# Kernel tuning notes

Hardware: AMD Instinct MI355X
Metric: run time of the kernel (lower is better)

The kernel has to match this reference:

```python
import jax, jax.numpy as jnp
import numpy as np

MAX_SPIKE_TIME = 100.0
TH = 1.0
BIT = 8
K = 3
PAD = 1
OUT_CH = 64


def _unfold3x3(x):
    # torch F.unfold(kernel=3, padding=1, stride=1): output (B, C*9, H*W),
    # feature order channel-major then (kh, kw).
    B, C, H, W = x.shape
    xp = jnp.pad(x, ((0, 0), (0, 0), (PAD, PAD), (PAD, PAD)))
    cols = [xp[:, :, i:i + H, j:j + W] for i in range(K) for j in range(K)]
    p = jnp.stack(cols, axis=2)            # (B, C, 9, H, W)
    return p.reshape(B, C * K * K, H * W)  # (B, C*9, L)


def _weight_quantization(w):
    # tanh -> scale by global abs-max (no grad through alpha) -> round with STE
    w = jnp.tanh(w)
    alpha = jax.lax.stop_gradient(jnp.max(jnp.abs(w)))
    qmax = float(2 ** (BIT - 1) - 1)
    w = jnp.clip(w / alpha, -1.0, 1.0) * qmax
    w_hat = jax.lax.stop_gradient(jnp.round(w) - w) + w
    return w_hat * alpha / qmax


def _t_linear_c(patches, weight):
    # patches: (B, L, F_in); weight: (F_out, F_in)
    sorted_inp = jnp.sort(patches, axis=-1)      # (B, L, F_in)
    indic = jnp.argsort(patches, axis=-1)        # (B, L, F_in)
    wT = weight.T                                # (F_in, F_out)
    w_sorted = wT[indic]                         # (B, L, F_in, F_out)
    wq = _weight_quantization(w_sorted)
    si = sorted_inp[..., None]                   # (B, L, F_in, 1)
    weight_input_mul = si * wq
    weight_sum = jnp.cumsum(wq, axis=-2)
    input_weight_sum = jnp.cumsum(weight_input_mul, axis=-2)
    out_all = input_weight_sum / jnp.clip(weight_sum - TH, 1e-10, 1e10)
    out_spike = jnp.where(weight_sum < TH, MAX_SPIKE_TIME, out_all)
    out_spike = jnp.where(out_spike < si, MAX_SPIKE_TIME, out_spike)
    # causality check against the NEXT sorted input time (1.0 for the last slot)
    next_in = jnp.concatenate([si[..., 1:, :], jnp.ones_like(si[..., :1, :])], axis=-2)
    out_spike = jnp.where(out_spike > next_in, MAX_SPIKE_TIME, out_spike)
    return jnp.min(out_spike, axis=-2)           # (B, L, F_out)


def setup_inputs() -> dict:
    key = jax.random.key(0)
    k1, k2 = jax.random.split(key)
    inp = jax.random.uniform(k1, (4, 16, 32, 32), dtype=jnp.float32)
    in_features = K * K * 16
    weight = jax.random.uniform(k2, (OUT_CH, in_features), dtype=jnp.float32) * (10.0 / in_features)
    return {"inp": inp, "weight": weight}


def reference(inp, weight):
    B, C, H, W = inp.shape
    patches = _unfold3x3(inp).transpose(0, 2, 1)          # (B, L, F_in)
    patches = jnp.where(patches < 0.1, MAX_SPIKE_TIME, patches)
    out = _t_linear_c(patches, weight)                    # (B, L, F_out)
    out = out.transpose(0, 2, 1).reshape(B, OUT_CH, H, W)  # stride=1, pad=1 -> same HW
    return out
```

## Files before the change

### kernel.cpp

```cpp
#include <hip/hip_runtime.h>
#include <math.h>

constexpr int F_IN   = 144;
constexpr int F_OUT  = 64;
constexpr int H_IMG  = 32;
constexpr int W_IMG  = 32;
constexpr int NPIX   = 4 * H_IMG * W_IMG;
constexpr int PPB    = 8;
constexpr int NTHR   = PPB * 64;
#define MAX_SPIKE 100.0f

__global__ __launch_bounds__(256) void quant_fused_kernel(
    const float* __restrict__ w,
    float* __restrict__ wqT)
{
#pragma clang fp contract(off)
    __shared__ float wred[4];
    const int tid = threadIdx.x;

    float m = 0.f;
    {
        const float4* w4 = (const float4*)w;
        for (int i = tid; i < (F_OUT * F_IN) / 4; i += 256) {
            const float4 v = w4[i];
            m = fmaxf(m, fmaxf(fmaxf(fabsf(v.x), fabsf(v.y)),
                               fmaxf(fabsf(v.z), fabsf(v.w))));
        }
    }
    for (int s = 32; s > 0; s >>= 1)
        m = fmaxf(m, __shfl_xor(m, s, 64));
    if ((tid & 63) == 0) wred[tid >> 6] = m;
    __syncthreads();
    const float mw = fmaxf(fmaxf(wred[0], wred[1]), fmaxf(wred[2], wred[3]));
    const float alpha = tanhf(mw);

    const int i = blockIdx.x * 256 + tid;
    const int o = i / F_IN;
    const int f = i - o * F_IN;
    const float t = tanhf(w[i]);
    float x = t / alpha;
    x = fminf(fmaxf(x, -1.f), 1.f) * 127.f;
    const float r = rintf(x);
    wqT[f * F_OUT + o] = r * alpha / 127.f;
}

__global__ __launch_bounds__(NTHR, 4) void spike_conv_kernel(
    const float* __restrict__ inp,
    const float* __restrict__ wq,
    float* __restrict__ out)
{
#pragma clang fp contract(off)
    __shared__ __align__(16) float wql[F_IN * F_OUT];
    __shared__ __align__(16) unsigned long long kr[PPB][F_IN];
    __shared__ float sv[PPB][F_IN + 1];

    const int tid  = threadIdx.x;
    const int lane = tid & 63;
    const int wv_i = tid >> 6;
    const int p    = blockIdx.x * PPB + wv_i;
    const int b    = p >> 10;
    const int l    = p & 1023;
    const int h    = l >> 5;
    const int w    = l & 31;

    for (int c = wv_i; c < 36; c += PPB) {
        const float* g = wq + c * 256 + lane * 4;
        __builtin_amdgcn_global_load_lds(
            (const __attribute__((address_space(1))) void*)g,
            (__attribute__((address_space(3))) void*)&wql[c * 256],
            16, 0, 0);
    }

    float v0f, v1f, v2f;
    unsigned long long key0, key1, key2;
    {
        int idx[3] = { lane, lane + 64, lane + 128 };
        float vals[3];
        for (int m = 0; m < 3; ++m) {
            const int i = idx[m];
            float v = MAX_SPIKE;
            if (i < F_IN) {
                const int c  = i / 9;
                const int r  = i - c * 9;
                const int kh = r / 3;
                const int kw = r - kh * 3;
                const int hh = h + kh - 1;
                const int ww = w + kw - 1;
                float x = 0.f;
                if (hh >= 0 && hh < H_IMG && ww >= 0 && ww < W_IMG)
                    x = inp[((b * 16 + c) * H_IMG + hh) * W_IMG + ww];
                v = (x < 0.1f) ? MAX_SPIKE : x;
                kr[wv_i][i] = ((unsigned long long)__float_as_uint(v) << 8)
                              | (unsigned)i;
            }
            vals[m] = v;
        }
        v0f = vals[0]; v1f = vals[1]; v2f = vals[2];
        key0 = ((unsigned long long)__float_as_uint(v0f) << 8) | (unsigned)idx[0];
        key1 = ((unsigned long long)__float_as_uint(v1f) << 8) | (unsigned)idx[1];
        key2 = ((unsigned long long)__float_as_uint(v2f) << 8) | (unsigned)idx[2];
        if (lane == 0) sv[wv_i][F_IN] = 1.0f;
    }

    int r0 = 0, r1 = 0, r2 = 0;
    {
        const ulonglong2* ks2 = (const ulonglong2*)&kr[wv_i][0];
#pragma unroll 4
        for (int j = 0; j < F_IN / 2; ++j) {
            const ulonglong2 kk = ks2[j];
            r0 += (kk.x < key0) + (kk.y < key0);
            r1 += (kk.x < key1) + (kk.y < key1);
            r2 += (kk.x < key2) + (kk.y < key2);
        }
    }

    {
        unsigned* krlo = (unsigned*)&kr[wv_i][0];
        sv[wv_i][r0] = v0f;  krlo[2 * r0] = (unsigned)lane << 6;
        sv[wv_i][r1] = v1f;  krlo[2 * r1] = (unsigned)(lane + 64) << 6;
        if (lane < F_IN - 128) {
            sv[wv_i][r2] = v2f;  krlo[2 * r2] = (unsigned)(lane + 128) << 6;
        }
    }

    {
        unsigned* krhi = (unsigned*)&kr[wv_i][0];
        for (int k = lane; k < F_IN; k += 64)
            krhi[2 * k + 1] = __float_as_uint(sv[wv_i][k + 1]);
    }

    __syncthreads();

    float s   = sv[wv_i][0];
    float ws  = 0.f;
    float iws = 0.f;
    float mn  = MAX_SPIKE;
    bool  done = false;
    const ulonglong2* rec2 = (const ulonglong2*)&kr[wv_i][0];
    for (int k0 = 0; k0 < F_IN; k0 += 8) {
        if (s >= MAX_SPIKE) break;
        const ulonglong2 ra = rec2[(k0 >> 1) + 0];
        const ulonglong2 rb = rec2[(k0 >> 1) + 1];
        const ulonglong2 rc = rec2[(k0 >> 1) + 2];
        const ulonglong2 rd = rec2[(k0 >> 1) + 3];
        const unsigned long long r8[8] = { ra.x, ra.y, rb.x, rb.y,
                                           rc.x, rc.y, rd.x, rd.y };
        float su[8], nx[8], wsu[8], iwsu[8];
#pragma unroll
        for (int u = 0; u < 8; ++u) {
            su[u] = s;
            nx[u] = __uint_as_float((unsigned)(r8[u] >> 32));
            const float wvv = wql[(unsigned)r8[u] + lane];
            ws += wvv;
            const float prod = su[u] * wvv;
            iws += prod;
            wsu[u]  = ws;
            iwsu[u] = iws;
            s = nx[u];
        }
        if (!__all(wsu[7] < 1.0f)) {
#pragma unroll
            for (int u = 0; u < 8; ++u) {
                const float d = fmaxf(wsu[u] - 1.0f, 1e-10f);
                const float q = iwsu[u] / d;
                const bool valid = (wsu[u] >= 1.0f) & (q >= su[u]) & (q <= nx[u]);
                if (valid & !done) { mn = q; done = true; }
            }
            if (__all(done)) break;
        }
    }
    out[(b * F_OUT + lane) * 1024 + l] = mn;
}

extern "C" void kernel_launch(void* const* d_in, const int* in_sizes, int n_in,
                              void* d_out, int out_size, void* d_ws, size_t ws_size,
                              hipStream_t stream) {
    const float* inp = (const float*)d_in[0];
    const float* w   = (const float*)d_in[1];
    float* out = (float*)d_out;
    float* wqT = (float*)d_ws;

    quant_fused_kernel<<<36, 256, 0, stream>>>(w, wqT);
    spike_conv_kernel<<<NPIX / PPB, NTHR, 0, stream>>>(inp, wqT, out);
}
```

Measured before the change: 80.06 us.

## Fuse weight quantization into spike conv kernel, recomputing per block

Removes the separate quantization kernel launch and its workspace round trip. Each block now loads the raw weights into registers (18 per thread), reduces the global abs-max across its waves, applies tanh, quantizes, and writes the transposed result into shared memory. This saves one launch and the dependency between kernels, but every one of the 512 blocks redoes the full weight tanh and quantization work and an extra block-wide reduction.

```diff
diff --git a/kernel.cpp b/kernel.cpp
--- a/kernel.cpp
+++ b/kernel.cpp
@@ -8,51 +8,19 @@
 constexpr int NPIX   = 4 * H_IMG * W_IMG;
 constexpr int PPB    = 8;
 constexpr int NTHR   = PPB * 64;
+constexpr int WPT    = F_IN / PPB;
 #define MAX_SPIKE 100.0f
 
-__global__ __launch_bounds__(256) void quant_fused_kernel(
+__global__ __launch_bounds__(NTHR, 4) void spike_conv_fused(
+    const float* __restrict__ inp,
     const float* __restrict__ w,
-    float* __restrict__ wqT)
-{
-#pragma clang fp contract(off)
-    __shared__ float wred[4];
-    const int tid = threadIdx.x;
-
-    float m = 0.f;
-    {
-        const float4* w4 = (const float4*)w;
-        for (int i = tid; i < (F_OUT * F_IN) / 4; i += 256) {
-            const float4 v = w4[i];
-            m = fmaxf(m, fmaxf(fmaxf(fabsf(v.x), fabsf(v.y)),
-                               fmaxf(fabsf(v.z), fabsf(v.w))));
-        }
-    }
-    for (int s = 32; s > 0; s >>= 1)
-        m = fmaxf(m, __shfl_xor(m, s, 64));
-    if ((tid & 63) == 0) wred[tid >> 6] = m;
-    __syncthreads();
-    const float mw = fmaxf(fmaxf(wred[0], wred[1]), fmaxf(wred[2], wred[3]));
-    const float alpha = tanhf(mw);
-
-    const int i = blockIdx.x * 256 + tid;
-    const int o = i / F_IN;
-    const int f = i - o * F_IN;
-    const float t = tanhf(w[i]);
-    float x = t / alpha;
-    x = fminf(fmaxf(x, -1.f), 1.f) * 127.f;
-    const float r = rintf(x);
-    wqT[f * F_OUT + o] = r * alpha / 127.f;
-}
-
-__global__ __launch_bounds__(NTHR, 4) void spike_conv_kernel(
-    const float* __restrict__ inp,
-    const float* __restrict__ wq,
     float* __restrict__ out)
 {
 #pragma clang fp contract(off)
     __shared__ __align__(16) float wql[F_IN * F_OUT];
     __shared__ __align__(16) unsigned long long kr[PPB][F_IN];
     __shared__ float sv[PPB][F_IN + 1];
+    __shared__ float wred[PPB];
 
     const int tid  = threadIdx.x;
     const int lane = tid & 63;
@@ -61,14 +29,18 @@
     const int b    = p >> 10;
     const int l    = p & 1023;
     const int h    = l >> 5;
-    const int w    = l & 31;
+    const int wcol = l & 31;
 
-    for (int c = wv_i; c < 36; c += PPB) {
-        const float* g = wq + c * 256 + lane * 4;
-        __builtin_amdgcn_global_load_lds(
-            (const __attribute__((address_space(1))) void*)g,
-            (__attribute__((address_space(3))) void*)&wql[c * 256],
-            16, 0, 0);
+    const int fbase = wv_i * WPT;
+    float wreg[WPT];
+    {
+        const float2* g2 = (const float2*)(w + lane * F_IN + fbase);
+#pragma unroll
+        for (int k2 = 0; k2 < WPT / 2; ++k2) {
+            const float2 v = g2[k2];
+            wreg[2 * k2]     = v.x;
+            wreg[2 * k2 + 1] = v.y;
+        }
     }
 
     float v0f, v1f, v2f;
@@ -76,8 +48,8 @@
     {
         int idx[3] = { lane, lane + 64, lane + 128 };
         float vals[3];
-        for (int m = 0; m < 3; ++m) {
-            const int i = idx[m];
+        for (int m2 = 0; m2 < 3; ++m2) {
+            const int i = idx[m2];
             float v = MAX_SPIKE;
             if (i < F_IN) {
                 const int c  = i / 9;
@@ -85,7 +57,7 @@
                 const int kh = r / 3;
                 const int kw = r - kh * 3;
                 const int hh = h + kh - 1;
-                const int ww = w + kw - 1;
+                const int ww = wcol + kw - 1;
                 float x = 0.f;
                 if (hh >= 0 && hh < H_IMG && ww >= 0 && ww < W_IMG)
                     x = inp[((b * 16 + c) * H_IMG + hh) * W_IMG + ww];
@@ -93,7 +65,7 @@
                 kr[wv_i][i] = ((unsigned long long)__float_as_uint(v) << 8)
                               | (unsigned)i;
             }
-            vals[m] = v;
+            vals[m2] = v;
         }
         v0f = vals[0]; v1f = vals[1]; v2f = vals[2];
         key0 = ((unsigned long long)__float_as_uint(v0f) << 8) | (unsigned)idx[0];
@@ -129,6 +101,26 @@
             krhi[2 * k + 1] = __float_as_uint(sv[wv_i][k + 1]);
     }
 
+    float m = 0.f;
+#pragma unroll
+    for (int k = 0; k < WPT; ++k) m = fmaxf(m, fabsf(wreg[k]));
+    for (int s = 32; s > 0; s >>= 1)
+        m = fmaxf(m, __shfl_xor(m, s, 64));
+    if (lane == 0) wred[wv_i] = m;
+    __syncthreads();
+    float mw = wred[0];
+#pragma unroll
+    for (int q = 1; q < PPB; ++q) mw = fmaxf(mw, wred[q]);
+    const float alpha = tanhf(mw);
+
+#pragma unroll
+    for (int k = 0; k < WPT; ++k) {
+        const float t = tanhf(wreg[k]);
+        float x = t / alpha;
+        x = fminf(fmaxf(x, -1.f), 1.f) * 127.f;
+        const float r = rintf(x);
+        wql[(fbase + k) * F_OUT + lane] = r * alpha / 127.f;
+    }
     __syncthreads();
 
     float s   = sv[wv_i][0];
@@ -178,8 +170,7 @@
     const float* inp = (const float*)d_in[0];
     const float* w   = (const float*)d_in[1];
     float* out = (float*)d_out;
-    float* wqT = (float*)d_ws;
+    (void)d_ws; (void)ws_size;
 
-    quant_fused_kernel<<<36, 256, 0, stream>>>(w, wqT);
-    spike_conv_kernel<<<NPIX / PPB, NTHR, 0, stream>>>(inp, wqT, out);
+    spike_conv_fused<<<NPIX / PPB, NTHR, 0, stream>>>(inp, w, out);
 }
```

Result: no change. 81.64 us (+2.0%).

## Read quantized weights from global/L1 instead of staging them in LDS

Applied to the files above, without the earlier changes.

The scan kernel no longer copies the 36 KB quantized weight matrix into shared memory per block. Weight lookups now read global memory directly, relying on L1/L2 caching of the small table. This removes the block-wide barrier and shrinks LDS use, so more blocks can stay resident. Pixels per block drop from 8 to 4 and the rank-counting loop is unrolled by hand. The cost is that the data-dependent gathers now have global-memory latency instead of LDS latency.

```diff
diff --git a/kernel.cpp b/kernel.cpp
--- a/kernel.cpp
+++ b/kernel.cpp
@@ -6,11 +6,11 @@
 constexpr int H_IMG  = 32;
 constexpr int W_IMG  = 32;
 constexpr int NPIX   = 4 * H_IMG * W_IMG;
-constexpr int PPB    = 8;
+constexpr int PPB    = 4;
 constexpr int NTHR   = PPB * 64;
 #define MAX_SPIKE 100.0f
 
-__global__ __launch_bounds__(256) void quant_fused_kernel(
+__global__ __launch_bounds__(256) void quant_kernel(
     const float* __restrict__ w,
     float* __restrict__ wqT)
 {
@@ -44,13 +44,12 @@
     wqT[f * F_OUT + o] = r * alpha / 127.f;
 }
 
-__global__ __launch_bounds__(NTHR, 4) void spike_conv_kernel(
+__global__ __launch_bounds__(NTHR, 4) void spike_scan_kernel(
     const float* __restrict__ inp,
     const float* __restrict__ wq,
     float* __restrict__ out)
 {
 #pragma clang fp contract(off)
-    __shared__ __align__(16) float wql[F_IN * F_OUT];
     __shared__ __align__(16) unsigned long long kr[PPB][F_IN];
     __shared__ float sv[PPB][F_IN + 1];
 
@@ -61,23 +60,15 @@
     const int b    = p >> 10;
     const int l    = p & 1023;
     const int h    = l >> 5;
-    const int w    = l & 31;
-
-    for (int c = wv_i; c < 36; c += PPB) {
-        const float* g = wq + c * 256 + lane * 4;
-        __builtin_amdgcn_global_load_lds(
-            (const __attribute__((address_space(1))) void*)g,
-            (__attribute__((address_space(3))) void*)&wql[c * 256],
-            16, 0, 0);
-    }
+    const int wcol = l & 31;
 
     float v0f, v1f, v2f;
     unsigned long long key0, key1, key2;
     {
         int idx[3] = { lane, lane + 64, lane + 128 };
         float vals[3];
-        for (int m = 0; m < 3; ++m) {
-            const int i = idx[m];
+        for (int m2 = 0; m2 < 3; ++m2) {
+            const int i = idx[m2];
             float v = MAX_SPIKE;
             if (i < F_IN) {
                 const int c  = i / 9;
@@ -85,7 +76,7 @@
                 const int kh = r / 3;
                 const int kw = r - kh * 3;
                 const int hh = h + kh - 1;
-                const int ww = w + kw - 1;
+                const int ww = wcol + kw - 1;
                 float x = 0.f;
                 if (hh >= 0 && hh < H_IMG && ww >= 0 && ww < W_IMG)
                     x = inp[((b * 16 + c) * H_IMG + hh) * W_IMG + ww];
@@ -93,7 +84,7 @@
                 kr[wv_i][i] = ((unsigned long long)__float_as_uint(v) << 8)
                               | (unsigned)i;
             }
-            vals[m] = v;
+            vals[m2] = v;
         }
         v0f = vals[0]; v1f = vals[1]; v2f = vals[2];
         key0 = ((unsigned long long)__float_as_uint(v0f) << 8) | (unsigned)idx[0];
@@ -105,12 +96,27 @@
     int r0 = 0, r1 = 0, r2 = 0;
     {
         const ulonglong2* ks2 = (const ulonglong2*)&kr[wv_i][0];
-#pragma unroll 4
-        for (int j = 0; j < F_IN / 2; ++j) {
-            const ulonglong2 kk = ks2[j];
-            r0 += (kk.x < key0) + (kk.y < key0);
-            r1 += (kk.x < key1) + (kk.y < key1);
-            r2 += (kk.x < key2) + (kk.y < key2);
+        for (int j = 0; j < F_IN / 2; j += 8) {
+            const ulonglong2 ka = ks2[j + 0];
+            const ulonglong2 kb = ks2[j + 1];
+            const ulonglong2 kc = ks2[j + 2];
+            const ulonglong2 kd = ks2[j + 3];
+            const ulonglong2 ke = ks2[j + 4];
+            const ulonglong2 kf = ks2[j + 5];
+            const ulonglong2 kg = ks2[j + 6];
+            const ulonglong2 kh2 = ks2[j + 7];
+            r0 += (ka.x < key0) + (ka.y < key0) + (kb.x < key0) + (kb.y < key0)
+                + (kc.x < key0) + (kc.y < key0) + (kd.x < key0) + (kd.y < key0)
+                + (ke.x < key0) + (ke.y < key0) + (kf.x < key0) + (kf.y < key0)
+                + (kg.x < key0) + (kg.y < key0) + (kh2.x < key0) + (kh2.y < key0);
+            r1 += (ka.x < key1) + (ka.y < key1) + (kb.x < key1) + (kb.y < key1)
+                + (kc.x < key1) + (kc.y < key1) + (kd.x < key1) + (kd.y < key1)
+                + (ke.x < key1) + (ke.y < key1) + (kf.x < key1) + (kf.y < key1)
+                + (kg.x < key1) + (kg.y < key1) + (kh2.x < key1) + (kh2.y < key1);
+            r2 += (ka.x < key2) + (ka.y < key2) + (kb.x < key2) + (kb.y < key2)
+                + (kc.x < key2) + (kc.y < key2) + (kd.x < key2) + (kd.y < key2)
+                + (ke.x < key2) + (ke.y < key2) + (kf.x < key2) + (kf.y < key2)
+                + (kg.x < key2) + (kg.y < key2) + (kh2.x < key2) + (kh2.y < key2);
         }
     }
 
@@ -128,8 +134,6 @@
         for (int k = lane; k < F_IN; k += 64)
             krhi[2 * k + 1] = __float_as_uint(sv[wv_i][k + 1]);
     }
-
-    __syncthreads();
 
     float s   = sv[wv_i][0];
     float ws  = 0.f;
@@ -150,7 +154,7 @@
         for (int u = 0; u < 8; ++u) {
             su[u] = s;
             nx[u] = __uint_as_float((unsigned)(r8[u] >> 32));
-            const float wvv = wql[(unsigned)r8[u] + lane];
+            const float wvv = wq[(unsigned)r8[u] + lane];
             ws += wvv;
             const float prod = su[u] * wvv;
             iws += prod;
@@ -180,6 +184,6 @@
     float* out = (float*)d_out;
     float* wqT = (float*)d_ws;
 
-    quant_fused_kernel<<<36, 256, 0, stream>>>(w, wqT);
-    spike_conv_kernel<<<NPIX / PPB, NTHR, 0, stream>>>(inp, wqT, out);
+    quant_kernel<<<36, 256, 0, stream>>>(w, wqT);
+    spike_scan_kernel<<<NPIX / PPB, NTHR, 0, stream>>>(inp, wqT, out);
 }
```

After: 82.43 us. 1.03x slower.

## Drop LDS weight staging, split rank sort across two waves per pixel

Applied to the files above, without the earlier changes.

Removes the per-block copy of the full 36KB quantized weight table into LDS. The scan now reads weights straight from global memory, relying on L1/L2 hits. Each pixel's rank-sort now uses two waves instead of one, and sorted values and offsets go into separate LDS arrays read as float4/uint4. With much less LDS per block, more blocks can run at once (launch bounds raised to 8), but the second wave per pixel sits idle during the scan and each gather now has global-memory latency.

```diff
diff --git a/kernel.cpp b/kernel.cpp
--- a/kernel.cpp
+++ b/kernel.cpp
@@ -6,11 +6,12 @@
 constexpr int H_IMG  = 32;
 constexpr int W_IMG  = 32;
 constexpr int NPIX   = 4 * H_IMG * W_IMG;
-constexpr int PPB    = 8;
-constexpr int NTHR   = PPB * 64;
+constexpr int PPB    = 4;
+constexpr int WPP    = 2;
+constexpr int NTHR   = PPB * WPP * 64;
 #define MAX_SPIKE 100.0f
 
-__global__ __launch_bounds__(256) void quant_fused_kernel(
+__global__ __launch_bounds__(256) void quant_kernel(
     const float* __restrict__ w,
     float* __restrict__ wqT)
 {
@@ -44,119 +45,108 @@
     wqT[f * F_OUT + o] = r * alpha / 127.f;
 }
 
-__global__ __launch_bounds__(NTHR, 4) void spike_conv_kernel(
+__global__ __launch_bounds__(NTHR, 8) void spike_scan_kernel(
     const float* __restrict__ inp,
     const float* __restrict__ wq,
     float* __restrict__ out)
 {
 #pragma clang fp contract(off)
-    __shared__ __align__(16) float wql[F_IN * F_OUT];
     __shared__ __align__(16) unsigned long long kr[PPB][F_IN];
-    __shared__ float sv[PPB][F_IN + 1];
+    __shared__ __align__(16) float svv[PPB][152];
+    __shared__ __align__(16) unsigned sof[PPB][F_IN];
 
     const int tid  = threadIdx.x;
     const int lane = tid & 63;
-    const int wv_i = tid >> 6;
-    const int p    = blockIdx.x * PPB + wv_i;
+    const int wave = tid >> 6;
+    const int pix  = wave >> 1;
+    const int half = wave & 1;
+    const int p    = blockIdx.x * PPB + pix;
     const int b    = p >> 10;
     const int l    = p & 1023;
     const int h    = l >> 5;
-    const int w    = l & 31;
+    const int wcol = l & 31;
 
-    for (int c = wv_i; c < 36; c += PPB) {
-        const float* g = wq + c * 256 + lane * 4;
-        __builtin_amdgcn_global_load_lds(
-            (const __attribute__((address_space(1))) void*)g,
-            (__attribute__((address_space(3))) void*)&wql[c * 256],
-            16, 0, 0);
+    const int f0 = half * 64 + lane;
+    const int f1 = 128 + half * 8 + lane;
+    const bool has1 = (lane < 8);
+    float v0, v1 = MAX_SPIKE;
+    {
+        const int c  = f0 / 9;
+        const int r  = f0 - c * 9;
+        const int kh = r / 3;
+        const int kw = r - kh * 3;
+        const int hh = h + kh - 1;
+        const int ww = wcol + kw - 1;
+        float x = 0.f;
+        if (hh >= 0 && hh < H_IMG && ww >= 0 && ww < W_IMG)
+            x = inp[((b * 16 + c) * H_IMG + hh) * W_IMG + ww];
+        v0 = (x < 0.1f) ? MAX_SPIKE : x;
+        kr[pix][f0] = ((unsigned long long)__float_as_uint(v0) << 8) | (unsigned)f0;
     }
+    if (has1) {
+        const int c  = f1 / 9;
+        const int r  = f1 - c * 9;
+        const int kh = r / 3;
+        const int kw = r - kh * 3;
+        const int hh = h + kh - 1;
+        const int ww = wcol + kw - 1;
+        float x = 0.f;
+        if (hh >= 0 && hh < H_IMG && ww >= 0 && ww < W_IMG)
+            x = inp[((b * 16 + c) * H_IMG + hh) * W_IMG + ww];
+        v1 = (x < 0.1f) ? MAX_SPIKE : x;
+        kr[pix][f1] = ((unsigned long long)__float_as_uint(v1) << 8) | (unsigned)f1;
+    }
+    const unsigned long long key0 =
+        ((unsigned long long)__float_as_uint(v0) << 8) | (unsigned)f0;
+    const unsigned long long key1 =
+        ((unsigned long long)__float_as_uint(v1) << 8) | (unsigned)f1;
+    if (half == 0 && lane == 0) svv[pix][F_IN] = 1.0f;
 
-    float v0f, v1f, v2f;
-    unsigned long long key0, key1, key2;
+    __syncthreads();
+
+    int r0 = 0, r1 = 0;
     {
-        int idx[3] = { lane, lane + 64, lane + 128 };
-        float vals[3];
-        for (int m = 0; m < 3; ++m) {
-            const int i = idx[m];
-            float v = MAX_SPIKE;
-            if (i < F_IN) {
-                const int c  = i / 9;
-                const int r  = i - c * 9;
-                const int kh = r / 3;
-                const int kw = r - kh * 3;
-                const int hh = h + kh - 1;
-                const int ww = w + kw - 1;
-                float x = 0.f;
-                if (hh >= 0 && hh < H_IMG && ww >= 0 && ww < W_IMG)
-                    x = inp[((b * 16 + c) * H_IMG + hh) * W_IMG + ww];
-                v = (x < 0.1f) ? MAX_SPIKE : x;
-                kr[wv_i][i] = ((unsigned long long)__float_as_uint(v) << 8)
-                              | (unsigned)i;
-            }
-            vals[m] = v;
-        }
-        v0f = vals[0]; v1f = vals[1]; v2f = vals[2];
-        key0 = ((unsigned long long)__float_as_uint(v0f) << 8) | (unsigned)idx[0];
-        key1 = ((unsigned long long)__float_as_uint(v1f) << 8) | (unsigned)idx[1];
-        key2 = ((unsigned long long)__float_as_uint(v2f) << 8) | (unsigned)idx[2];
-        if (lane == 0) sv[wv_i][F_IN] = 1.0f;
-    }
-
-    int r0 = 0, r1 = 0, r2 = 0;
-    {
-        const ulonglong2* ks2 = (const ulonglong2*)&kr[wv_i][0];
+        const ulonglong2* ks2 = (const ulonglong2*)&kr[pix][0];
 #pragma unroll 4
         for (int j = 0; j < F_IN / 2; ++j) {
             const ulonglong2 kk = ks2[j];
             r0 += (kk.x < key0) + (kk.y < key0);
             r1 += (kk.x < key1) + (kk.y < key1);
-            r2 += (kk.x < key2) + (kk.y < key2);
         }
     }
 
-    {
-        unsigned* krlo = (unsigned*)&kr[wv_i][0];
-        sv[wv_i][r0] = v0f;  krlo[2 * r0] = (unsigned)lane << 6;
-        sv[wv_i][r1] = v1f;  krlo[2 * r1] = (unsigned)(lane + 64) << 6;
-        if (lane < F_IN - 128) {
-            sv[wv_i][r2] = v2f;  krlo[2 * r2] = (unsigned)(lane + 128) << 6;
-        }
-    }
-
-    {
-        unsigned* krhi = (unsigned*)&kr[wv_i][0];
-        for (int k = lane; k < F_IN; k += 64)
-            krhi[2 * k + 1] = __float_as_uint(sv[wv_i][k + 1]);
-    }
+    svv[pix][r0] = v0;  sof[pix][r0] = (unsigned)f0 << 6;
+    if (has1) { svv[pix][r1] = v1;  sof[pix][r1] = (unsigned)f1 << 6; }
 
     __syncthreads();
 
-    float s   = sv[wv_i][0];
+    if (half != 0) return;
+
+    float s   = svv[pix][0];
     float ws  = 0.f;
     float iws = 0.f;
     float mn  = MAX_SPIKE;
     bool  done = false;
-    const ulonglong2* rec2 = (const ulonglong2*)&kr[wv_i][0];
     for (int k0 = 0; k0 < F_IN; k0 += 8) {
         if (s >= MAX_SPIKE) break;
-        const ulonglong2 ra = rec2[(k0 >> 1) + 0];
-        const ulonglong2 rb = rec2[(k0 >> 1) + 1];
-        const ulonglong2 rc = rec2[(k0 >> 1) + 2];
-        const ulonglong2 rd = rec2[(k0 >> 1) + 3];
-        const unsigned long long r8[8] = { ra.x, ra.y, rb.x, rb.y,
-                                           rc.x, rc.y, rd.x, rd.y };
+        const float4 sa = *(const float4*)&svv[pix][k0];
+        const float4 sb = *(const float4*)&svv[pix][k0 + 4];
+        const float nxt8 = svv[pix][k0 + 8];
+        const uint4  oa = *(const uint4*)&sof[pix][k0];
+        const uint4  ob = *(const uint4*)&sof[pix][k0 + 4];
+        const float    sv8[8] = { sa.x, sa.y, sa.z, sa.w, sb.x, sb.y, sb.z, sb.w };
+        const unsigned o8[8]  = { oa.x, oa.y, oa.z, oa.w, ob.x, ob.y, ob.z, ob.w };
         float su[8], nx[8], wsu[8], iwsu[8];
 #pragma unroll
         for (int u = 0; u < 8; ++u) {
-            su[u] = s;
-            nx[u] = __uint_as_float((unsigned)(r8[u] >> 32));
-            const float wvv = wql[(unsigned)r8[u] + lane];
+            su[u] = sv8[u];
+            nx[u] = (u < 7) ? sv8[u + 1] : nxt8;
+            const float wvv = wq[o8[u] + lane];
             ws += wvv;
             const float prod = su[u] * wvv;
             iws += prod;
             wsu[u]  = ws;
             iwsu[u] = iws;
-            s = nx[u];
         }
         if (!__all(wsu[7] < 1.0f)) {
 #pragma unroll
@@ -168,6 +158,7 @@
             }
             if (__all(done)) break;
         }
+        s = nxt8;
     }
     out[(b * F_OUT + lane) * 1024 + l] = mn;
 }
@@ -180,6 +171,6 @@
     float* out = (float*)d_out;
     float* wqT = (float*)d_ws;
 
-    quant_fused_kernel<<<36, 256, 0, stream>>>(w, wqT);
-    spike_conv_kernel<<<NPIX / PPB, NTHR, 0, stream>>>(inp, wqT, out);
+    quant_kernel<<<36, 256, 0, stream>>>(w, wqT);
+    spike_scan_kernel<<<NPIX / PPB, NTHR, 0, stream>>>(inp, wqT, out);
 }
```

Result: slower. 84.69 us (+5.8%).
